# Kernel optimization log

Hardware: AMD Instinct MI355X
Metric: run time of the kernel (lower is better)

The kernel has to match this reference:

```python
import jax, jax.numpy as jnp
import numpy as np

LN_EPS = 1e-5
LOG_EPS = 1e-8

def _layernorm(x, w, b):
    mu = jnp.mean(x, axis=-1, keepdims=True)
    var = jnp.mean((x - mu) ** 2, axis=-1, keepdims=True)
    return (x - mu) * jax.lax.rsqrt(var + LN_EPS) * w + b


def setup_inputs() -> dict:
    key = jax.random.key(0)
    ks = jax.random.split(key, 8)
    B, T, D = 4, 4096, 1024
    x = jax.random.normal(ks[0], (B, T, D), dtype=jnp.float32)
    ln_w = jnp.ones((D,), jnp.float32)
    ln_b = jnp.zeros((D,), jnp.float32)
    # torch Linear stores weight as (out, in)
    Wf = jax.random.normal(ks[1], (D, D), jnp.float32) / np.sqrt(D)
    bf = jax.random.normal(ks[2], (D,), jnp.float32) * 0.02
    # module inits reach to zeros; use small random values for a non-trivial baseline
    Wr = jax.random.normal(ks[3], (D, D), jnp.float32) * 0.02
    br = jax.random.normal(ks[4], (D,), jnp.float32) * 0.02
    alpha_bias = jnp.array([3.0], jnp.float32) + jax.random.normal(ks[5], (1,), jnp.float32) * 0.1
    beta_scale = jnp.array([0.02], jnp.float32)
    return {"x": x, "ln_w": ln_w, "ln_b": ln_b, "Wf": Wf, "bf": bf,
            "Wr": Wr, "br": br, "alpha_bias": alpha_bias, "beta_scale": beta_scale}


def reference(x, ln_w, ln_b, Wf, bf, Wr, br, alpha_bias, beta_scale):
    residual = x
    x_norm = _layernorm(x, ln_w, ln_b)                       # [B,T,D]
    alpha = jax.nn.sigmoid(jnp.einsum('btd,ed->bte', x_norm, Wf) + bf + alpha_bias)
    beta_x = beta_scale * (1.0 - alpha) * x_norm
    log_alpha = jnp.log(alpha + LOG_EPS)
    log_alpha_cumsum = jnp.cumsum(log_alpha, axis=1)          # [B,T,D]
    m = jnp.max(log_alpha_cumsum, axis=1, keepdims=True)      # [B,1,D]
    scale = jnp.exp(log_alpha_cumsum - m)
    x_star = beta_x * scale
    s_star = jnp.cumsum(x_star, axis=1)
    output = s_star / (scale + LOG_EPS)
    x_gate = jnp.tanh(jnp.einsum('btd,ed->bte', output, Wr) + br)
    return x_gate * 0.05 + residual
```

## Files before the change

### kernel.cpp

```cpp
#include <hip/hip_runtime.h>

#define D_DIM 1024
#define B_DIM 4
#define T_DIM 4096
#define M_DIM (B_DIM * T_DIM)
#define CHUNK 32
#define NCHUNK (T_DIM / CHUNK)
#define NWAVE_C 16
#define SEG (NCHUNK / NWAVE_C)
#define NKT (D_DIM / 64)

typedef unsigned short u16;
typedef __attribute__((ext_vector_type(8))) __bf16 bf16x8;
typedef __attribute__((ext_vector_type(4))) float f32x4;

__device__ __forceinline__ float bf2f(u16 u) {
    union { unsigned int i; float f; } v;
    v.i = ((unsigned int)u) << 16;
    return v.f;
}
__device__ __forceinline__ u16 f2bf(float f) {
    union { float f; unsigned int i; } v;
    v.f = f;
    unsigned int u = v.i;
    unsigned int r = (u + 0x7fffu + ((u >> 16) & 1u)) >> 16;
    return (u16)r;
}
__device__ __forceinline__ float fast_tanh(float v) {
    float e = __expf(2.f * v);
    return 1.f - 2.f / (e + 1.f);
}

#define GLOAD16(g, l)                                                   \
    __builtin_amdgcn_global_load_lds(                                   \
        (const __attribute__((address_space(1))) void*)(g),             \
        (__attribute__((address_space(3))) void*)(l), 16, 0, 0)

#define BAR()                                      \
    do {                                           \
        __builtin_amdgcn_sched_barrier(0);         \
        asm volatile("" ::: "memory");             \
        __builtin_amdgcn_s_barrier();              \
        asm volatile("" ::: "memory");             \
        __builtin_amdgcn_sched_barrier(0);         \
    } while (0)

#define WAITVM(N) asm volatile("s_waitcnt vmcnt(" #N ")" ::: "memory")

__global__ __launch_bounds__(256) void ln_conv_kernel(const float* __restrict__ x,
                                                      const float* __restrict__ w,
                                                      const float* __restrict__ b,
                                                      u16* __restrict__ xn,
                                                      const float* __restrict__ Wf,
                                                      const float* __restrict__ Wr,
                                                      u16* __restrict__ da,
                                                      u16* __restrict__ db) {
    int tid = threadIdx.x;
    if (blockIdx.x < 2048) {
        int i = blockIdx.x * 256 + tid;
        const float* s = (i < 262144) ? Wf : Wr;
        u16* dp = (i < 262144) ? da : db;
        int j = i & 262143;
        float4 v = ((const float4*)s)[j];
        ushort4 o;
        o.x = f2bf(v.x); o.y = f2bf(v.y); o.z = f2bf(v.z); o.w = f2bf(v.w);
        ((ushort4*)dp)[j] = o;
        return;
    }
    int wv = tid >> 6, lane = tid & 63;
    int row = (blockIdx.x - 2048) * 4 + wv;
    const float4* xr = (const float4*)(x + (size_t)row * D_DIM);
    float4 xv[4];
    #pragma unroll
    for (int k = 0; k < 4; k++) xv[k] = xr[lane + 64 * k];
    float s = 0.f, s2 = 0.f;
    #pragma unroll
    for (int k = 0; k < 4; k++) {
        s  += xv[k].x + xv[k].y + xv[k].z + xv[k].w;
        s2 += xv[k].x * xv[k].x + xv[k].y * xv[k].y
            + xv[k].z * xv[k].z + xv[k].w * xv[k].w;
    }
    #pragma unroll
    for (int o = 1; o < 64; o <<= 1) {
        s  += __shfl_xor(s, o, 64);
        s2 += __shfl_xor(s2, o, 64);
    }
    float mu = s * (1.0f / D_DIM);
    float var = s2 * (1.0f / D_DIM) - mu * mu;
    float rs = rsqrtf(var + 1e-5f);
    ushort4* xo = (ushort4*)(xn + (size_t)row * D_DIM);
    #pragma unroll
    for (int k = 0; k < 4; k++) {
        float4 wv4 = ((const float4*)w)[lane + 64 * k];
        float4 bv4 = ((const float4*)b)[lane + 64 * k];
        ushort4 o;
        o.x = f2bf((xv[k].x - mu) * rs * wv4.x + bv4.x);
        o.y = f2bf((xv[k].y - mu) * rs * wv4.y + bv4.y);
        o.z = f2bf((xv[k].z - mu) * rs * wv4.z + bv4.z);
        o.w = f2bf((xv[k].w - mu) * rs * wv4.w + bv4.w);
        xo[lane + 64 * k] = o;
    }
}

__device__ __forceinline__ void gemm256_core(const u16* __restrict__ AG,
                                             const u16* __restrict__ BG,
                                             int tile_m, int tile_n,
                                             u16* ldsA, u16* ldsB,
                                             f32x4 (*acc)[4]) {
    int tid  = threadIdx.x;
    int wave = tid >> 6, lane = tid & 63;
    int wr = wave >> 2, wc = wave & 3;
    int q = lane >> 4;
    int srow = tid >> 3;
    int scol = ((tid & 7) ^ (srow & 7)) * 8;
    const u16* gA = AG + (size_t)(tile_m + srow) * D_DIM + scol;
    const u16* gB = BG + (size_t)(tile_n + srow) * D_DIM + scol;
    int ldst = wave * 512;
    int aRow = wr * 128 + (lane & 15);
    int bRow = wc * 64 + (lane & 15);
    int x7 = lane & 7;
    int s0 = (q ^ x7) * 8;
    int s1 = ((4 | q) ^ x7) * 8;

#define STG4(ldsbase, gsrc, koff)                                        \
    do {                                                                 \
        _Pragma("unroll") for (int j = 0; j < 4; j++)                    \
            GLOAD16((gsrc) + (size_t)j * (64 * D_DIM) + (koff),          \
                    (ldsbase) + j * 4096 + ldst);                        \
    } while (0)

#define MMQ(Af, Bf, mo, no)                                              \
    do {                                                                 \
        __builtin_amdgcn_s_setprio(1);                                   \
        _Pragma("unroll") for (int mi_ = 0; mi_ < 4; mi_++)              \
            _Pragma("unroll") for (int ni_ = 0; ni_ < 2; ni_++) {        \
                acc[(mo) + mi_][(no) + ni_] =                            \
                    __builtin_amdgcn_mfma_f32_16x16x32_bf16(             \
                        Af[mi_][0], Bf[ni_][0],                          \
                        acc[(mo) + mi_][(no) + ni_], 0, 0, 0);           \
                acc[(mo) + mi_][(no) + ni_] =                            \
                    __builtin_amdgcn_mfma_f32_16x16x32_bf16(             \
                        Af[mi_][1], Bf[ni_][1],                          \
                        acc[(mo) + mi_][(no) + ni_], 0, 0, 0);           \
            }                                                            \
        __builtin_amdgcn_s_setprio(0);                                   \
    } while (0)

    STG4(ldsA, gA, 0);
    STG4(ldsB, gB, 0);
    STG4(ldsA + 16384, gA, 64);
    STG4(ldsB + 16384, gB, 64);
    WAITVM(8);
    BAR();

    for (int t = 0; t < NKT; t++) {
        int c = t & 1;
        const u16* pA = ldsA + c * 16384 + aRow * 64;
        const u16* pB = ldsB + c * 16384 + bRow * 64;
        bf16x8 A0[4][2], A1[4][2], B0[2][2], B1[2][2];
        #pragma unroll
        for (int mi = 0; mi < 4; mi++) {
            A0[mi][0] = *(const bf16x8*)(pA + mi * 1024 + s0);
            A0[mi][1] = *(const bf16x8*)(pA + mi * 1024 + s1);
        }
        #pragma unroll
        for (int ni = 0; ni < 2; ni++) {
            B0[ni][0] = *(const bf16x8*)(pB + ni * 1024 + s0);
            B0[ni][1] = *(const bf16x8*)(pB + ni * 1024 + s1);
        }
        MMQ(A0, B0, 0, 0);
        #pragma unroll
        for (int mi = 0; mi < 4; mi++) {
            A1[mi][0] = *(const bf16x8*)(pA + (mi + 4) * 1024 + s0);
            A1[mi][1] = *(const bf16x8*)(pA + (mi + 4) * 1024 + s1);
        }
        #pragma unroll
        for (int ni = 0; ni < 2; ni++) {
            B1[ni][0] = *(const bf16x8*)(pB + (ni + 2) * 1024 + s0);
            B1[ni][1] = *(const bf16x8*)(pB + (ni + 2) * 1024 + s1);
        }
        MMQ(A0, B1, 0, 2);
        BAR();
        if (t + 2 < NKT) STG4(ldsA + c * 16384, gA, (size_t)(t + 2) * 64);
        MMQ(A1, B0, 4, 0);
        if (t + 2 < NKT) {
            STG4(ldsB + c * 16384, gB, (size_t)(t + 2) * 64);
            WAITVM(8);
        } else {
            WAITVM(0);
        }
        BAR();
        MMQ(A1, B1, 4, 2);
    }
#undef STG4
#undef MMQ
}

__global__ __launch_bounds__(512, 2) void gemm1_kernel(const u16* __restrict__ xn,
                                                       const u16* __restrict__ Wfc,
                                                       const float* __restrict__ bf_,
                                                       const float* __restrict__ ab,
                                                       const float* __restrict__ bs,
                                                       u16* __restrict__ out_la,
                                                       float* __restrict__ Sg,
                                                       float* __restrict__ Tg) {
    __shared__ __align__(16) u16 ldsA[2][16384];
    __shared__ __align__(16) u16 ldsB[2][16384];
    int flat = blockIdx.y * 4 + blockIdx.x;
    int xcd = flat & 7, p = flat >> 3;
    int tile_m = (xcd * 8 + (p >> 2)) * 256;
    int tile_n = (p & 3) * 256;
    f32x4 acc[8][4] = {};
    gemm256_core(xn, Wfc, tile_m, tile_n, &ldsA[0][0], &ldsB[0][0], acc);

    int tid = threadIdx.x, wave = tid >> 6, lane = tid & 63;
    int wr = wave >> 2, wc = wave & 3;
    float abv = ab[0], bsv = bs[0];
    int q = lane >> 4, l = lane & 15;
    #pragma unroll
    for (int ni = 0; ni < 4; ni++) {
        int col = tile_n + wc * 64 + ni * 16 + l;
        float bcol = bf_[col];
        #pragma unroll
        for (int ch = 0; ch < 4; ch++) {
            float lav[2][4], bxv[2][4];
            #pragma unroll
            for (int h = 0; h < 2; h++) {
                int mi = 2 * ch + h;
                #pragma unroll
                for (int r = 0; r < 4; r++) {
                    int row = tile_m + wr * 128 + mi * 16 + q * 4 + r;
                    float z = acc[mi][ni][r] + bcol + abv;
                    float alpha = 1.f / (1.f + __expf(-z));
                    float la_ = __logf(alpha + 1e-8f);
                    float xv = bf2f(xn[(size_t)row * D_DIM + col]);
                    lav[h][r] = la_;
                    bxv[h][r] = bsv * (1.f - alpha) * xv;
                    out_la[(size_t)row * D_DIM + col] = f2bf(la_);
                }
            }
            float s0 = lav[0][0] + lav[0][1] + lav[0][2] + lav[0][3];
            float s1 = lav[1][0] + lav[1][1] + lav[1][2] + lav[1][3];
            float x0 = s0, x1 = s1, y;
            y = __shfl_up(x0, 16, 64); if (q >= 1) x0 += y;
            y = __shfl_up(x0, 32, 64); if (q >= 2) x0 += y;
            y = __shfl_up(x1, 16, 64); if (q >= 1) x1 += y;
            y = __shfl_up(x1, 32, 64); if (q >= 2) x1 += y;
            float t0 = __shfl(x0, l + 48, 64);
            float t1 = __shfl(x1, l + 48, 64);
            float e0 = x0 - s0, e1 = x1 - s1;
            float pr = e0, Tp = 0.f;
            #pragma unroll
            for (int r = 0; r < 4; r++) { pr += lav[0][r]; Tp += bxv[0][r] * __expf(pr); }
            pr = t0 + e1;
            #pragma unroll
            for (int r = 0; r < 4; r++) { pr += lav[1][r]; Tp += bxv[1][r] * __expf(pr); }
            Tp += __shfl_xor(Tp, 16, 64);
            Tp += __shfl_xor(Tp, 32, 64);
            if (q == 0) {
                int cidx = ((tile_m + wr * 128) >> 5) + ch;
                Sg[(size_t)cidx * D_DIM + col] = t0 + t1;
                Tg[(size_t)cidx * D_DIM + col] = Tp;
            }
        }
    }
}

__global__ __launch_bounds__(1024) void scan_combine(const u16* __restrict__ la,
                                                     const float* __restrict__ S,
                                                     const float* __restrict__ Tb,
                                                     float* __restrict__ Of,
                                                     float* __restrict__ SSp) {
    __shared__ float lsS[NWAVE_C][64], lsW[NWAVE_C][64];
    int b = blockIdx.x >> 4;
    int dg = blockIdx.x & 15;
    int wave = threadIdx.x >> 6, lane = threadIdx.x & 63;
    int d = dg * 64 + lane;
    float m = bf2f(la[(size_t)(b * T_DIM) * D_DIM + d]);
    size_t base = ((size_t)b * NCHUNK) * D_DIM + d;
    int c0 = wave * SEG;

    float OfR[SEG], wR[SEG];
    float Or = 0.f, w = 0.f;
    #pragma unroll
    for (int j = 0; j < SEG; j++) {
        size_t ci = base + (size_t)(c0 + j) * D_DIM;
        OfR[j] = Or;
        wR[j]  = w;
        w  += __expf(Or) * Tb[ci];
        Or += S[ci];
    }
    lsS[wave][lane] = Or; lsW[wave][lane] = w;
    __syncthreads();

    float o = 0.f, s = 0.f, myO = 0.f, myS = 0.f;
    #pragma unroll
    for (int w2 = 0; w2 < NWAVE_C; w2++) {
        if (w2 == wave) { myO = o; myS = s; }
        s += __expf(o - m) * lsW[w2][lane];
        o += lsS[w2][lane];
    }

    float em = __expf(myO - m);
    #pragma unroll
    for (int j = 0; j < SEG; j++) {
        size_t ci = base + (size_t)(c0 + j) * D_DIM;
        Of[ci]  = myO + OfR[j] - m;
        SSp[ci] = myS + em * wR[j];
    }
}

__global__ __launch_bounds__(256) void scan_final(const u16* __restrict__ la,
                                                  const u16* __restrict__ xn,
                                                  const float* __restrict__ bs,
                                                  const float* __restrict__ Of,
                                                  const float* __restrict__ SSp,
                                                  u16* __restrict__ osc) {
    int bc = blockIdx.x;
    int b = bc >> 7, c = bc & (NCHUNK - 1);
    int col0 = threadIdx.x * 4;
    float bsv = bs[0];
    size_t base = ((size_t)(b * T_DIM + c * CHUNK)) * D_DIM + col0;
    size_t ci = ((size_t)(b * NCHUNK + c)) * D_DIM + col0;
    float ofs[4], ss[4], p[4];
    #pragma unroll
    for (int j = 0; j < 4; j++) { ofs[j] = Of[ci + j]; ss[j] = SSp[ci + j]; p[j] = 0.f; }
    #pragma unroll 8
    for (int t = 0; t < CHUNK; t++) {
        size_t idx = base + (size_t)t * D_DIM;
        ushort4 lv = *(const ushort4*)(la + idx);
        ushort4 xv = *(const ushort4*)(xn + idx);
        u16 lvs[4] = {lv.x, lv.y, lv.z, lv.w};
        u16 xvs[4] = {xv.x, xv.y, xv.z, xv.w};
        u16 os[4];
        #pragma unroll
        for (int j = 0; j < 4; j++) {
            float lav = bf2f(lvs[j]);
            p[j] += lav;
            float scv = __expf(ofs[j] + p[j]);
            float bx = bsv * (1.f - __expf(lav)) * bf2f(xvs[j]);
            ss[j] += bx * scv;
            os[j] = f2bf(ss[j] / (scv + 1e-8f));
        }
        ushort4 o; o.x = os[0]; o.y = os[1]; o.z = os[2]; o.w = os[3];
        *(ushort4*)(osc + idx) = o;
    }
}

__global__ __launch_bounds__(512, 2) void gemm2_kernel(const u16* __restrict__ A,
                                                       const u16* __restrict__ Bm,
                                                       const float* __restrict__ bias,
                                                       const float* __restrict__ resid,
                                                       float* __restrict__ out_f) {
    __shared__ __align__(16) u16 ldsA[2][16384];
    __shared__ __align__(16) u16 ldsB[2][16384];
    int flat = blockIdx.y * 4 + blockIdx.x;
    int xcd = flat & 7, p = flat >> 3;
    int tile_m = (xcd * 8 + (p >> 2)) * 256;
    int tile_n = (p & 3) * 256;
    f32x4 acc[8][4] = {};
    gemm256_core(A, Bm, tile_m, tile_n, &ldsA[0][0], &ldsB[0][0], acc);

    int tid = threadIdx.x, wave = tid >> 6, lane = tid & 63;
    int wr = wave >> 2, wc = wave & 3;
    int q = lane >> 4, l = lane & 15;
    #pragma unroll
    for (int mi = 0; mi < 8; mi++) {
        #pragma unroll
        for (int r = 0; r < 4; r++) {
            int row = tile_m + wr * 128 + mi * 16 + q * 4 + r;
            #pragma unroll
            for (int ni = 0; ni < 4; ni++) {
                int col = tile_n + wc * 64 + ni * 16 + l;
                size_t idx = (size_t)row * D_DIM + col;
                float g = fast_tanh(acc[mi][ni][r] + bias[col]);
                out_f[idx] = 0.05f * g + resid[idx];
            }
        }
    }
}

extern "C" void kernel_launch(void* const* d_in, const int* in_sizes, int n_in,
                              void* d_out, int out_size, void* d_ws, size_t ws_size,
                              hipStream_t stream) {
    const float* x   = (const float*)d_in[0];
    const float* lnw = (const float*)d_in[1];
    const float* lnb = (const float*)d_in[2];
    const float* Wf  = (const float*)d_in[3];
    const float* bf_ = (const float*)d_in[4];
    const float* Wr  = (const float*)d_in[5];
    const float* br  = (const float*)d_in[6];
    const float* ab  = (const float*)d_in[7];
    const float* bs  = (const float*)d_in[8];
    float* out = (float*)d_out;

    char* w = (char*)d_ws;
    u16* xn  = (u16*)w;
    u16* la  = (u16*)(w + (size_t)33554432);
    u16* Wfc = (u16*)(w + (size_t)67108864);
    u16* Wrc = (u16*)(w + (size_t)69206016);
    float* S   = (float*)(w + (size_t)71303168);
    float* Tb  = S  + 524288;
    float* Of  = Tb + 524288;
    float* SSp = Of + 524288;
    u16* osc = xn;

    ln_conv_kernel<<<dim3(2048 + M_DIM / 4), dim3(256), 0, stream>>>(
        x, lnw, lnb, xn, Wf, Wr, Wfc, Wrc);
    gemm1_kernel<<<dim3(D_DIM / 256, M_DIM / 256), dim3(512), 0, stream>>>(
        xn, Wfc, bf_, ab, bs, la, S, Tb);
    scan_combine<<<dim3(B_DIM * 16), dim3(1024), 0, stream>>>(la, S, Tb, Of, SSp);
    scan_final<<<dim3(B_DIM * NCHUNK), dim3(256), 0, stream>>>(la, xn, bs, Of, SSp, osc);
    gemm2_kernel<<<dim3(D_DIM / 256, M_DIM / 256), dim3(512), 0, stream>>>(
        osc, Wrc, br, x, out);
}
```

Before: 274.0 us.

## Restructure GEMM main loop into explicit ping-pong schedule with barriers between phases

New measurement: 395.1 us. +44.2%, slower.

```diff
diff --git a/kernel.cpp b/kernel.cpp
--- a/kernel.cpp
+++ b/kernel.cpp
@@ -46,6 +46,11 @@
     } while (0)
 
 #define WAITVM(N) asm volatile("s_waitcnt vmcnt(" #N ")" ::: "memory")
+#define LGKM0()                                    \
+    do {                                           \
+        asm volatile("s_waitcnt lgkmcnt(0)" ::: "memory"); \
+        __builtin_amdgcn_sched_barrier(0);         \
+    } while (0)
 
 __global__ __launch_bounds__(256) void ln_conv_kernel(const float* __restrict__ x,
                                                       const float* __restrict__ w,
@@ -129,22 +134,40 @@
                     (ldsbase) + j * 4096 + ldst);                        \
     } while (0)
 
+#define RD_A(dst, base, mo)                                              \
+    do {                                                                 \
+        _Pragma("unroll") for (int mi_ = 0; mi_ < 4; mi_++) {            \
+            dst[mi_][0] = *(const bf16x8*)((base) + ((mo) + mi_) * 1024 + s0); \
+            dst[mi_][1] = *(const bf16x8*)((base) + ((mo) + mi_) * 1024 + s1); \
+        }                                                                \
+    } while (0)
+
+#define RD_B(dst, base, no)                                              \
+    do {                                                                 \
+        _Pragma("unroll") for (int ni_ = 0; ni_ < 2; ni_++) {            \
+            dst[ni_][0] = *(const bf16x8*)((base) + ((no) + ni_) * 1024 + s0); \
+            dst[ni_][1] = *(const bf16x8*)((base) + ((no) + ni_) * 1024 + s1); \
+        }                                                                \
+    } while (0)
+
 #define MMQ(Af, Bf, mo, no)                                              \
     do {                                                                 \
         __builtin_amdgcn_s_setprio(1);                                   \
-        _Pragma("unroll") for (int mi_ = 0; mi_ < 4; mi_++)              \
-            _Pragma("unroll") for (int ni_ = 0; ni_ < 2; ni_++) {        \
-                acc[(mo) + mi_][(no) + ni_] =                            \
-                    __builtin_amdgcn_mfma_f32_16x16x32_bf16(             \
-                        Af[mi_][0], Bf[ni_][0],                          \
-                        acc[(mo) + mi_][(no) + ni_], 0, 0, 0);           \
-                acc[(mo) + mi_][(no) + ni_] =                            \
-                    __builtin_amdgcn_mfma_f32_16x16x32_bf16(             \
-                        Af[mi_][1], Bf[ni_][1],                          \
-                        acc[(mo) + mi_][(no) + ni_], 0, 0, 0);           \
-            }                                                            \
+        _Pragma("unroll") for (int ks_ = 0; ks_ < 2; ks_++)              \
+            _Pragma("unroll") for (int mi_ = 0; mi_ < 4; mi_++)          \
+                _Pragma("unroll") for (int ni_ = 0; ni_ < 2; ni_++)      \
+                    acc[(mo) + mi_][(no) + ni_] =                        \
+                        __builtin_amdgcn_mfma_f32_16x16x32_bf16(         \
+                            Af[mi_][ks_], Bf[ni_][ks_],                  \
+                            acc[(mo) + mi_][(no) + ni_], 0, 0, 0);       \
         __builtin_amdgcn_s_setprio(0);                                   \
     } while (0)
+
+    const u16* pA0 = ldsA + aRow * 64;
+    const u16* pA1 = ldsA + 16384 + aRow * 64;
+    const u16* pB0 = ldsB + bRow * 64;
+    const u16* pB1 = ldsB + 16384 + bRow * 64;
+    bf16x8 A0[4][2], A1[4][2], B0[2][2], B1[2][2];
 
     STG4(ldsA, gA, 0);
     STG4(ldsB, gB, 0);
@@ -153,46 +176,57 @@
     WAITVM(8);
     BAR();
 
-    for (int t = 0; t < NKT; t++) {
-        int c = t & 1;
-        const u16* pA = ldsA + c * 16384 + aRow * 64;
-        const u16* pB = ldsB + c * 16384 + bRow * 64;
-        bf16x8 A0[4][2], A1[4][2], B0[2][2], B1[2][2];
-        #pragma unroll
-        for (int mi = 0; mi < 4; mi++) {
-            A0[mi][0] = *(const bf16x8*)(pA + mi * 1024 + s0);
-            A0[mi][1] = *(const bf16x8*)(pA + mi * 1024 + s1);
-        }
-        #pragma unroll
-        for (int ni = 0; ni < 2; ni++) {
-            B0[ni][0] = *(const bf16x8*)(pB + ni * 1024 + s0);
-            B0[ni][1] = *(const bf16x8*)(pB + ni * 1024 + s1);
-        }
+    for (int i = 0; i < NKT / 2; i++) {
+        RD_A(A0, pA0, 0);
+        RD_B(B0, pB0, 0);
+        BAR(); LGKM0();
         MMQ(A0, B0, 0, 0);
-        #pragma unroll
-        for (int mi = 0; mi < 4; mi++) {
-            A1[mi][0] = *(const bf16x8*)(pA + (mi + 4) * 1024 + s0);
-            A1[mi][1] = *(const bf16x8*)(pA + (mi + 4) * 1024 + s1);
-        }
-        #pragma unroll
-        for (int ni = 0; ni < 2; ni++) {
-            B1[ni][0] = *(const bf16x8*)(pB + (ni + 2) * 1024 + s0);
-            B1[ni][1] = *(const bf16x8*)(pB + (ni + 2) * 1024 + s1);
-        }
+        BAR();
+        RD_B(B1, pB0, 2);
+        BAR(); LGKM0();
         MMQ(A0, B1, 0, 2);
         BAR();
-        if (t + 2 < NKT) STG4(ldsA + c * 16384, gA, (size_t)(t + 2) * 64);
-        MMQ(A1, B0, 4, 0);
-        if (t + 2 < NKT) {
-            STG4(ldsB + c * 16384, gB, (size_t)(t + 2) * 64);
+        RD_A(A1, pA0, 4);
+        BAR(); LGKM0();
+        MMQ(A1, B1, 4, 2);
+        BAR();
+        if (i + 1 < NKT / 2) {
+            STG4(ldsA, gA, (size_t)(2 * i + 2) * 64);
+            STG4(ldsB, gB, (size_t)(2 * i + 2) * 64);
             WAITVM(8);
         } else {
             WAITVM(0);
         }
         BAR();
+        MMQ(A1, B0, 4, 0);
+        BAR();
+        RD_A(A0, pA1, 0);
+        RD_B(B0, pB1, 0);
+        BAR(); LGKM0();
+        MMQ(A0, B0, 0, 0);
+        BAR();
+        RD_B(B1, pB1, 2);
+        BAR(); LGKM0();
+        MMQ(A0, B1, 0, 2);
+        BAR();
+        RD_A(A1, pA1, 4);
+        BAR(); LGKM0();
         MMQ(A1, B1, 4, 2);
+        BAR();
+        if (i + 1 < NKT / 2) {
+            STG4(ldsA + 16384, gA, (size_t)(2 * i + 3) * 64);
+            STG4(ldsB + 16384, gB, (size_t)(2 * i + 3) * 64);
+            WAITVM(8);
+        } else {
+            WAITVM(0);
+        }
+        BAR();
+        MMQ(A1, B0, 4, 0);
+        BAR();
     }
 #undef STG4
+#undef RD_A
+#undef RD_B
 #undef MMQ
 }
 
```
